# Performance work log

Hardware: AMD Instinct MI355X
Metric: run time of the kernel (lower is better)

## Reference

```python
import jax, jax.numpy as jnp
import numpy as np

TAU = 0.05
SIGMA = 0.05
THETA = 1.0
MAX_ITER = 30
B, N, M1, M2 = 8192, 256, 128, 64


def setup_inputs() -> dict:
    key = jax.random.key(0)
    k = jax.random.split(key, 5)
    x0 = jax.random.normal(k[0], (B, N), dtype=jnp.float32)
    y1_0 = jnp.zeros((B, M1), dtype=jnp.float32)
    y2_0 = jnp.zeros((B, M2), dtype=jnp.float32)
    z = jax.random.normal(k[1], (B, M1 + M2), dtype=jnp.float32)
    c = jax.random.normal(k[2], (N,), dtype=jnp.float32)
    # scale constraint matrices so tau*sigma*||A||^2 < 1 (PDHG stability)
    A1 = jax.random.normal(k[3], (M1, N), dtype=jnp.float32) * 0.1
    A2 = jax.random.normal(k[4], (M2, N), dtype=jnp.float32) * 0.1
    return {"x0": x0, "y1_0": y1_0, "y2_0": y2_0, "z": z, "c": c, "A1": A1, "A2": A2}


def reference(x0, y1_0, y2_0, z, c, A1, A2):
    # affine constraint maps: ineq_map(x, z) = x @ A1^T - z1 ; eq_map(x, z) = x @ A2^T - z2
    # adjoints: A1^T y1 = y1 @ A1 ; A2^T y2 = y2 @ A2
    # prox: projection onto nonnegative orthant
    z1, z2 = z[:, :M1], z[:, M1:]

    def step(carry, _):
        x, x_bar, y1, y2 = carry
        y1 = jnp.maximum(y1 + SIGMA * (x_bar @ A1.T - z1), 0.0)   # dual ineq ascent + clamp
        y2 = y2 + SIGMA * (x_bar @ A2.T - z2)                     # dual eq ascent
        grad = c + y1 @ A1 + y2 @ A2                              # [B, N] via broadcast of c
        x_next = jnp.maximum(x - TAU * grad, 0.0)                 # prox (nonneg projection)
        x_bar = x_next + THETA * (x_next - x)                     # extrapolation
        return (x_next, x_bar, y1, y2), None

    (x, _, y1, y2), _ = jax.lax.scan(step, (x0, x0, y1_0, y2_0), None, length=MAX_ITER)
    return (x, y1, y2)
```

## Files before the change

kernel.cpp:

```cpp
#include <hip/hip_runtime.h>

typedef __attribute__((ext_vector_type(8))) __bf16 bf16x8;
typedef __attribute__((ext_vector_type(4))) float f32x4;
typedef __attribute__((ext_vector_type(4))) int i32x4;

constexpr int Bn = 8192, Nn = 256, M1n = 128, M2n = 64, Mn = 192, ITERS = 30;
constexpr float TAUc = 0.05f, SIGc = 0.05f;

__device__ __forceinline__ ushort f2bf(float f) {
  unsigned u = __builtin_bit_cast(unsigned, f);
  u = (u + 0x7FFFu + ((u >> 16) & 1u)) >> 16;
  return (ushort)u;
}

__device__ __forceinline__ unsigned cvtpk(float lo, float hi) {
  unsigned r;
  asm("v_cvt_pk_bf16_f32 %0, %1, %2" : "=v"(r) : "v"(lo), "v"(hi));
  return r;
}

__device__ __forceinline__ void pina(i32x4& v) { asm volatile("" : "+a"(v)); }

__device__ __forceinline__ f32x4 mfma_b(bf16x8 a, i32x4 bfrag, f32x4 acc) {
  return __builtin_amdgcn_mfma_f32_16x16x32_bf16(
      a, __builtin_bit_cast(bf16x8, bfrag), acc, 0, 0, 0);
}

__global__ void prep_kernel(const float* __restrict__ A1, const float* __restrict__ A2,
                            ushort* __restrict__ Arm, ushort* __restrict__ AT) {
  int i = blockIdx.x * 256 + threadIdx.x;
  if (i >= Mn * Nn) return;
  int m = i / Nn, n = i % Nn;
  float v = (m < M1n) ? A1[m * Nn + n] : A2[(m - M1n) * Nn + n];
  ushort b = f2bf(v);
  Arm[m * Nn + n] = b;
  AT[n * Mn + m] = b;
}

__global__ __launch_bounds__(512, 2) void pdhg_kernel(
    const float* __restrict__ x0, const float* __restrict__ y10,
    const float* __restrict__ y20, const float* __restrict__ z,
    const float* __restrict__ c, const ushort* __restrict__ Arm,
    const ushort* __restrict__ AT, float* __restrict__ out) {
  __shared__ __align__(16) ushort xb_lds[2][16][264];
  __shared__ __align__(16) ushort y_lds[2][16][200];

  const int lane = threadIdx.x & 63;
  const int w = threadIdx.x >> 6;
  const int fr = lane & 15;
  const int kg = lane >> 4;
  const int row0 = blockIdx.x * 32;

  const int m01 = w * 16 + fr;
  const int m2 = M1n + (w & 3) * 16 + fr;
  const int bu2 = w >> 2;
  const int nA = (2 * w) * 16 + fr;
  const int nB = (2 * w + 1) * 16 + fr;

  float x[2][2][4];
  float yu[3][4], zu[3][4];
  const float cvA = c[nA], cvB = c[nB];

#pragma unroll
  for (int t = 0; t < 2; ++t) {
    const int n = t ? nB : nA;
#pragma unroll
    for (int b = 0; b < 2; ++b)
#pragma unroll
      for (int g = 0; g < 4; ++g) {
        float v = x0[(row0 + 16 * b + kg * 4 + g) * Nn + n];
        x[t][b][g] = v;
        xb_lds[b][kg * 4 + g][n] = f2bf(v);
      }
  }
#pragma unroll
  for (int g = 0; g < 4; ++g) {
    int r0 = row0 + kg * 4 + g;
    int r1 = r0 + 16;
    int r2 = row0 + 16 * bu2 + kg * 4 + g;
    zu[0][g] = SIGc * z[r0 * Mn + m01];  yu[0][g] = y10[r0 * M1n + m01];
    zu[1][g] = SIGc * z[r1 * Mn + m01];  yu[1][g] = y10[r1 * M1n + m01];
    zu[2][g] = SIGc * z[r2 * Mn + m2];   yu[2][g] = y20[r2 * M2n + (m2 - M1n)];
  }

  i32x4 armF01[8], armF2[8], atFA[6], atFB[6];
#pragma unroll
  for (int kf = 0; kf < 8; ++kf) {
    armF01[kf] = *reinterpret_cast<const i32x4*>(&Arm[m01 * Nn + kf * 32 + kg * 8]); pina(armF01[kf]);
    armF2[kf]  = *reinterpret_cast<const i32x4*>(&Arm[m2 * Nn + kf * 32 + kg * 8]);  pina(armF2[kf]);
  }
#pragma unroll
  for (int kf = 0; kf < 6; ++kf) {
    atFA[kf] = *reinterpret_cast<const i32x4*>(&AT[nA * Mn + kf * 32 + kg * 8]); pina(atFA[kf]);
    atFB[kf] = *reinterpret_cast<const i32x4*>(&AT[nB * Mn + kf * 32 + kg * 8]); pina(atFB[kf]);
  }

  __syncthreads();

  for (int it = 0; it < ITERS; ++it) {
    f32x4 a0 = {0.f, 0.f, 0.f, 0.f}, a1 = a0, a2 = a0;
#pragma unroll
    for (int kf = 0; kf < 8; ++kf) {
      bf16x8 f0 = *reinterpret_cast<const bf16x8*>(&xb_lds[0][fr][kf * 32 + kg * 8]);
      bf16x8 f1 = *reinterpret_cast<const bf16x8*>(&xb_lds[1][fr][kf * 32 + kg * 8]);
      bf16x8 f2 = *reinterpret_cast<const bf16x8*>(&xb_lds[bu2][fr][kf * 32 + kg * 8]);
      a0 = mfma_b(f0, armF01[kf], a0);
      a1 = mfma_b(f1, armF01[kf], a1);
      a2 = mfma_b(f2, armF2[kf], a2);
    }

#pragma unroll
    for (int g = 0; g < 4; ++g) {
      yu[0][g] = fmaxf(__builtin_fmaf(SIGc, a0[g], yu[0][g]) - zu[0][g], 0.f);
      yu[1][g] = fmaxf(__builtin_fmaf(SIGc, a1[g], yu[1][g]) - zu[1][g], 0.f);
      yu[2][g] = __builtin_fmaf(SIGc, a2[g], yu[2][g]) - zu[2][g];
    }
    {
      unsigned p01 = cvtpk(yu[0][0], yu[0][1]), p23 = cvtpk(yu[0][2], yu[0][3]);
      y_lds[0][kg * 4 + 0][m01] = (ushort)p01;
      y_lds[0][kg * 4 + 1][m01] = (ushort)(p01 >> 16);
      y_lds[0][kg * 4 + 2][m01] = (ushort)p23;
      y_lds[0][kg * 4 + 3][m01] = (ushort)(p23 >> 16);
    }
    {
      unsigned p01 = cvtpk(yu[1][0], yu[1][1]), p23 = cvtpk(yu[1][2], yu[1][3]);
      y_lds[1][kg * 4 + 0][m01] = (ushort)p01;
      y_lds[1][kg * 4 + 1][m01] = (ushort)(p01 >> 16);
      y_lds[1][kg * 4 + 2][m01] = (ushort)p23;
      y_lds[1][kg * 4 + 3][m01] = (ushort)(p23 >> 16);
    }
    {
      unsigned p01 = cvtpk(yu[2][0], yu[2][1]), p23 = cvtpk(yu[2][2], yu[2][3]);
      y_lds[bu2][kg * 4 + 0][m2] = (ushort)p01;
      y_lds[bu2][kg * 4 + 1][m2] = (ushort)(p01 >> 16);
      y_lds[bu2][kg * 4 + 2][m2] = (ushort)p23;
      y_lds[bu2][kg * 4 + 3][m2] = (ushort)(p23 >> 16);
    }
    __syncthreads();

    f32x4 b00 = {0.f, 0.f, 0.f, 0.f}, b01 = b00, b10 = b00, b11 = b00;
#pragma unroll
    for (int kf = 0; kf < 6; ++kf) {
      bf16x8 g0 = *reinterpret_cast<const bf16x8*>(&y_lds[0][fr][kf * 32 + kg * 8]);
      bf16x8 g1 = *reinterpret_cast<const bf16x8*>(&y_lds[1][fr][kf * 32 + kg * 8]);
      b00 = mfma_b(g0, atFA[kf], b00);
      b01 = mfma_b(g0, atFB[kf], b01);
      b10 = mfma_b(g1, atFA[kf], b10);
      b11 = mfma_b(g1, atFB[kf], b11);
    }

    const bool notlast = (it != ITERS - 1);
#pragma unroll
    for (int t = 0; t < 2; ++t) {
      const int n = t ? nB : nA;
      const float cv = t ? cvB : cvA;
#pragma unroll
      for (int b = 0; b < 2; ++b) {
        const f32x4 bt = (t == 0) ? (b == 0 ? b00 : b10) : (b == 0 ? b01 : b11);
        float xb[4];
#pragma unroll
        for (int g = 0; g < 4; ++g) {
          float grad = cv + bt[g];
          float xn = fmaxf(__builtin_fmaf(-TAUc, grad, x[t][b][g]), 0.f);
          xb[g] = 2.f * xn - x[t][b][g];
          x[t][b][g] = xn;
        }
        if (notlast) {
          unsigned p01 = cvtpk(xb[0], xb[1]), p23 = cvtpk(xb[2], xb[3]);
          xb_lds[b][kg * 4 + 0][n] = (ushort)p01;
          xb_lds[b][kg * 4 + 1][n] = (ushort)(p01 >> 16);
          xb_lds[b][kg * 4 + 2][n] = (ushort)p23;
          xb_lds[b][kg * 4 + 3][n] = (ushort)(p23 >> 16);
        }
      }
    }
    if (notlast) __syncthreads();
  }

  float* ox = out;
  float* oy1 = out + Bn * Nn;
  float* oy2 = oy1 + Bn * M1n;
#pragma unroll
  for (int t = 0; t < 2; ++t) {
    const int n = t ? nB : nA;
#pragma unroll
    for (int b = 0; b < 2; ++b)
#pragma unroll
      for (int g = 0; g < 4; ++g)
        ox[(row0 + 16 * b + kg * 4 + g) * Nn + n] = x[t][b][g];
  }
#pragma unroll
  for (int g = 0; g < 4; ++g) {
    int r0 = row0 + kg * 4 + g;
    oy1[r0 * M1n + m01] = yu[0][g];
    oy1[(r0 + 16) * M1n + m01] = yu[1][g];
    oy2[(row0 + 16 * bu2 + kg * 4 + g) * M2n + (m2 - M1n)] = yu[2][g];
  }
}

extern "C" void kernel_launch(void* const* d_in, const int* in_sizes, int n_in,
                              void* d_out, int out_size, void* d_ws, size_t ws_size,
                              hipStream_t stream) {
  const float* x0  = (const float*)d_in[0];
  const float* y10 = (const float*)d_in[1];
  const float* y20 = (const float*)d_in[2];
  const float* z   = (const float*)d_in[3];
  const float* c   = (const float*)d_in[4];
  const float* A1  = (const float*)d_in[5];
  const float* A2  = (const float*)d_in[6];

  ushort* Arm = (ushort*)d_ws;
  ushort* AT  = Arm + Mn * Nn;

  prep_kernel<<<(Mn * Nn + 255) / 256, 256, 0, stream>>>(A1, A2, Arm, AT);
  pdhg_kernel<<<Bn / 32, 512, 0, stream>>>(x0, y10, y20, z, c, Arm, AT, (float*)d_out);
}
```

Measured before the change: 74.13 us.

## Swap MFMA operands so outputs are row-contiguous and vectorize LDS/global I/O

Swaps the MFMA A/B operands so the register-resident A-matrix fragments are the A operand and the activations are B. Each lane's accumulator then holds four consecutive columns of one batch row instead of four rows of one column. This lets LDS writes of x_bar and y become single 8-byte stores instead of four 2-byte scattered stores, and makes the initial loads and final stores 16-byte vectors. It also changes the warp work split to 3 M-tiles by 1 batch tile in the first GEMM, which reduces redundant LDS reads of x_bar. Bank conflicts from the new row-strided store pattern are a possible risk.

```diff
diff --git a/kernel.cpp b/kernel.cpp
--- a/kernel.cpp
+++ b/kernel.cpp
@@ -21,9 +21,9 @@
 
 __device__ __forceinline__ void pina(i32x4& v) { asm volatile("" : "+a"(v)); }
 
-__device__ __forceinline__ f32x4 mfma_b(bf16x8 a, i32x4 bfrag, f32x4 acc) {
+__device__ __forceinline__ f32x4 mfma_swp(i32x4 afrag, bf16x8 b, f32x4 acc) {
   return __builtin_amdgcn_mfma_f32_16x16x32_bf16(
-      a, __builtin_bit_cast(bf16x8, bfrag), acc, 0, 0, 0);
+      __builtin_bit_cast(bf16x8, afrag), b, acc, 0, 0, 0);
 }
 
 __global__ void prep_kernel(const float* __restrict__ A1, const float* __restrict__ A2,
@@ -51,48 +51,56 @@
   const int kg = lane >> 4;
   const int row0 = blockIdx.x * 32;
 
-  const int m01 = w * 16 + fr;
-  const int m2 = M1n + (w & 3) * 16 + fr;
-  const int bu2 = w >> 2;
-  const int nA = (2 * w) * 16 + fr;
-  const int nB = (2 * w + 1) * 16 + fr;
+  const int b1 = w & 1;
+  const int mg = w >> 1;
+  const int rG1 = row0 + 16 * b1 + fr;
 
   float x[2][2][4];
-  float yu[3][4], zu[3][4];
-  const float cvA = c[nA], cvB = c[nB];
+  float cv[2][4];
+  float ys[3][4], zs[3][4];
 
 #pragma unroll
   for (int t = 0; t < 2; ++t) {
-    const int n = t ? nB : nA;
-#pragma unroll
-    for (int b = 0; b < 2; ++b)
-#pragma unroll
-      for (int g = 0; g < 4; ++g) {
-        float v = x0[(row0 + 16 * b + kg * 4 + g) * Nn + n];
-        x[t][b][g] = v;
-        xb_lds[b][kg * 4 + g][n] = f2bf(v);
-      }
-  }
-#pragma unroll
-  for (int g = 0; g < 4; ++g) {
-    int r0 = row0 + kg * 4 + g;
-    int r1 = r0 + 16;
-    int r2 = row0 + 16 * bu2 + kg * 4 + g;
-    zu[0][g] = SIGc * z[r0 * Mn + m01];  yu[0][g] = y10[r0 * M1n + m01];
-    zu[1][g] = SIGc * z[r1 * Mn + m01];  yu[1][g] = y10[r1 * M1n + m01];
-    zu[2][g] = SIGc * z[r2 * Mn + m2];   yu[2][g] = y20[r2 * M2n + (m2 - M1n)];
-  }
-
-  i32x4 armF01[8], armF2[8], atFA[6], atFB[6];
-#pragma unroll
-  for (int kf = 0; kf < 8; ++kf) {
-    armF01[kf] = *reinterpret_cast<const i32x4*>(&Arm[m01 * Nn + kf * 32 + kg * 8]); pina(armF01[kf]);
-    armF2[kf]  = *reinterpret_cast<const i32x4*>(&Arm[m2 * Nn + kf * 32 + kg * 8]);  pina(armF2[kf]);
-  }
-#pragma unroll
-  for (int kf = 0; kf < 6; ++kf) {
-    atFA[kf] = *reinterpret_cast<const i32x4*>(&AT[nA * Mn + kf * 32 + kg * 8]); pina(atFA[kf]);
-    atFB[kf] = *reinterpret_cast<const i32x4*>(&AT[nB * Mn + kf * 32 + kg * 8]); pina(atFB[kf]);
+    const int n0 = (2 * w + t) * 16 + kg * 4;
+    *reinterpret_cast<f32x4*>(cv[t]) = *reinterpret_cast<const f32x4*>(&c[n0]);
+#pragma unroll
+    for (int b = 0; b < 2; ++b) {
+      f32x4 v = *reinterpret_cast<const f32x4*>(&x0[(row0 + 16 * b + fr) * Nn + n0]);
+#pragma unroll
+      for (int g = 0; g < 4; ++g) x[t][b][g] = v[g];
+      uint2 p = make_uint2(cvtpk(v[0], v[1]), cvtpk(v[2], v[3]));
+      *reinterpret_cast<uint2*>(&xb_lds[b][fr][n0]) = p;
+    }
+  }
+#pragma unroll
+  for (int i = 0; i < 3; ++i) {
+    const int mt = 3 * mg + i;
+    const int m0 = mt * 16 + kg * 4;
+    f32x4 zv = *reinterpret_cast<const f32x4*>(&z[rG1 * Mn + m0]);
+    f32x4 yv = (mt < 8) ? *reinterpret_cast<const f32x4*>(&y10[rG1 * M1n + m0])
+                        : *reinterpret_cast<const f32x4*>(&y20[rG1 * M2n + (m0 - M1n)]);
+#pragma unroll
+    for (int g = 0; g < 4; ++g) { zs[i][g] = SIGc * zv[g]; ys[i][g] = yv[g]; }
+  }
+
+  i32x4 armF[3][8], atF[2][6];
+#pragma unroll
+  for (int i = 0; i < 3; ++i) {
+    const int m = (3 * mg + i) * 16 + fr;
+#pragma unroll
+    for (int kf = 0; kf < 8; ++kf) {
+      armF[i][kf] = *reinterpret_cast<const i32x4*>(&Arm[m * Nn + kf * 32 + kg * 8]);
+      pina(armF[i][kf]);
+    }
+  }
+#pragma unroll
+  for (int t = 0; t < 2; ++t) {
+    const int n = (2 * w + t) * 16 + fr;
+#pragma unroll
+    for (int kf = 0; kf < 6; ++kf) {
+      atF[t][kf] = *reinterpret_cast<const i32x4*>(&AT[n * Mn + kf * 32 + kg * 8]);
+      pina(atF[t][kf]);
+    }
   }
 
   __syncthreads();
@@ -101,76 +109,57 @@
     f32x4 a0 = {0.f, 0.f, 0.f, 0.f}, a1 = a0, a2 = a0;
 #pragma unroll
     for (int kf = 0; kf < 8; ++kf) {
-      bf16x8 f0 = *reinterpret_cast<const bf16x8*>(&xb_lds[0][fr][kf * 32 + kg * 8]);
-      bf16x8 f1 = *reinterpret_cast<const bf16x8*>(&xb_lds[1][fr][kf * 32 + kg * 8]);
-      bf16x8 f2 = *reinterpret_cast<const bf16x8*>(&xb_lds[bu2][fr][kf * 32 + kg * 8]);
-      a0 = mfma_b(f0, armF01[kf], a0);
-      a1 = mfma_b(f1, armF01[kf], a1);
-      a2 = mfma_b(f2, armF2[kf], a2);
-    }
-
-#pragma unroll
-    for (int g = 0; g < 4; ++g) {
-      yu[0][g] = fmaxf(__builtin_fmaf(SIGc, a0[g], yu[0][g]) - zu[0][g], 0.f);
-      yu[1][g] = fmaxf(__builtin_fmaf(SIGc, a1[g], yu[1][g]) - zu[1][g], 0.f);
-      yu[2][g] = __builtin_fmaf(SIGc, a2[g], yu[2][g]) - zu[2][g];
-    }
-    {
-      unsigned p01 = cvtpk(yu[0][0], yu[0][1]), p23 = cvtpk(yu[0][2], yu[0][3]);
-      y_lds[0][kg * 4 + 0][m01] = (ushort)p01;
-      y_lds[0][kg * 4 + 1][m01] = (ushort)(p01 >> 16);
-      y_lds[0][kg * 4 + 2][m01] = (ushort)p23;
-      y_lds[0][kg * 4 + 3][m01] = (ushort)(p23 >> 16);
-    }
-    {
-      unsigned p01 = cvtpk(yu[1][0], yu[1][1]), p23 = cvtpk(yu[1][2], yu[1][3]);
-      y_lds[1][kg * 4 + 0][m01] = (ushort)p01;
-      y_lds[1][kg * 4 + 1][m01] = (ushort)(p01 >> 16);
-      y_lds[1][kg * 4 + 2][m01] = (ushort)p23;
-      y_lds[1][kg * 4 + 3][m01] = (ushort)(p23 >> 16);
-    }
-    {
-      unsigned p01 = cvtpk(yu[2][0], yu[2][1]), p23 = cvtpk(yu[2][2], yu[2][3]);
-      y_lds[bu2][kg * 4 + 0][m2] = (ushort)p01;
-      y_lds[bu2][kg * 4 + 1][m2] = (ushort)(p01 >> 16);
-      y_lds[bu2][kg * 4 + 2][m2] = (ushort)p23;
-      y_lds[bu2][kg * 4 + 3][m2] = (ushort)(p23 >> 16);
+      bf16x8 fx = *reinterpret_cast<const bf16x8*>(&xb_lds[b1][fr][kf * 32 + kg * 8]);
+      a0 = mfma_swp(armF[0][kf], fx, a0);
+      a1 = mfma_swp(armF[1][kf], fx, a1);
+      a2 = mfma_swp(armF[2][kf], fx, a2);
+    }
+
+#pragma unroll
+    for (int i = 0; i < 3; ++i) {
+      const int mt = 3 * mg + i;
+      const int m0 = mt * 16 + kg * 4;
+      const f32x4 ai = (i == 0) ? a0 : (i == 1) ? a1 : a2;
+      const bool relu = (mt < 8);
+#pragma unroll
+      for (int g = 0; g < 4; ++g) {
+        float s = __builtin_fmaf(SIGc, ai[g], ys[i][g]) - zs[i][g];
+        ys[i][g] = relu ? fmaxf(s, 0.f) : s;
+      }
+      uint2 p = make_uint2(cvtpk(ys[i][0], ys[i][1]), cvtpk(ys[i][2], ys[i][3]));
+      *reinterpret_cast<uint2*>(&y_lds[b1][fr][m0]) = p;
     }
     __syncthreads();
 
-    f32x4 b00 = {0.f, 0.f, 0.f, 0.f}, b01 = b00, b10 = b00, b11 = b00;
+    f32x4 q00 = {0.f, 0.f, 0.f, 0.f}, q01 = q00, q10 = q00, q11 = q00;
 #pragma unroll
     for (int kf = 0; kf < 6; ++kf) {
       bf16x8 g0 = *reinterpret_cast<const bf16x8*>(&y_lds[0][fr][kf * 32 + kg * 8]);
       bf16x8 g1 = *reinterpret_cast<const bf16x8*>(&y_lds[1][fr][kf * 32 + kg * 8]);
-      b00 = mfma_b(g0, atFA[kf], b00);
-      b01 = mfma_b(g0, atFB[kf], b01);
-      b10 = mfma_b(g1, atFA[kf], b10);
-      b11 = mfma_b(g1, atFB[kf], b11);
+      q00 = mfma_swp(atF[0][kf], g0, q00);
+      q01 = mfma_swp(atF[1][kf], g0, q01);
+      q10 = mfma_swp(atF[0][kf], g1, q10);
+      q11 = mfma_swp(atF[1][kf], g1, q11);
     }
 
     const bool notlast = (it != ITERS - 1);
 #pragma unroll
     for (int t = 0; t < 2; ++t) {
-      const int n = t ? nB : nA;
-      const float cv = t ? cvB : cvA;
+      const int n0 = (2 * w + t) * 16 + kg * 4;
 #pragma unroll
       for (int b = 0; b < 2; ++b) {
-        const f32x4 bt = (t == 0) ? (b == 0 ? b00 : b10) : (b == 0 ? b01 : b11);
+        const f32x4 qt = (t == 0) ? (b == 0 ? q00 : q10) : (b == 0 ? q01 : q11);
         float xb[4];
 #pragma unroll
         for (int g = 0; g < 4; ++g) {
-          float grad = cv + bt[g];
+          float grad = cv[t][g] + qt[g];
           float xn = fmaxf(__builtin_fmaf(-TAUc, grad, x[t][b][g]), 0.f);
           xb[g] = 2.f * xn - x[t][b][g];
           x[t][b][g] = xn;
         }
         if (notlast) {
-          unsigned p01 = cvtpk(xb[0], xb[1]), p23 = cvtpk(xb[2], xb[3]);
-          xb_lds[b][kg * 4 + 0][n] = (ushort)p01;
-          xb_lds[b][kg * 4 + 1][n] = (ushort)(p01 >> 16);
-          xb_lds[b][kg * 4 + 2][n] = (ushort)p23;
-          xb_lds[b][kg * 4 + 3][n] = (ushort)(p23 >> 16);
+          uint2 p = make_uint2(cvtpk(xb[0], xb[1]), cvtpk(xb[2], xb[3]));
+          *reinterpret_cast<uint2*>(&xb_lds[b][fr][n0]) = p;
         }
       }
     }
@@ -182,19 +171,24 @@
   float* oy2 = oy1 + Bn * M1n;
 #pragma unroll
   for (int t = 0; t < 2; ++t) {
-    const int n = t ? nB : nA;
-#pragma unroll
-    for (int b = 0; b < 2; ++b)
-#pragma unroll
-      for (int g = 0; g < 4; ++g)
-        ox[(row0 + 16 * b + kg * 4 + g) * Nn + n] = x[t][b][g];
-  }
-#pragma unroll
-  for (int g = 0; g < 4; ++g) {
-    int r0 = row0 + kg * 4 + g;
-    oy1[r0 * M1n + m01] = yu[0][g];
-    oy1[(r0 + 16) * M1n + m01] = yu[1][g];
-    oy2[(row0 + 16 * bu2 + kg * 4 + g) * M2n + (m2 - M1n)] = yu[2][g];
+    const int n0 = (2 * w + t) * 16 + kg * 4;
+#pragma unroll
+    for (int b = 0; b < 2; ++b) {
+      f32x4 v;
+#pragma unroll
+      for (int g = 0; g < 4; ++g) v[g] = x[t][b][g];
+      *reinterpret_cast<f32x4*>(&ox[(row0 + 16 * b + fr) * Nn + n0]) = v;
+    }
+  }
+#pragma unroll
+  for (int i = 0; i < 3; ++i) {
+    const int mt = 3 * mg + i;
+    const int m0 = mt * 16 + kg * 4;
+    f32x4 v;
+#pragma unroll
+    for (int g = 0; g < 4; ++g) v[g] = ys[i][g];
+    if (mt < 8) *reinterpret_cast<f32x4*>(&oy1[rG1 * M1n + m0]) = v;
+    else        *reinterpret_cast<f32x4*>(&oy2[rG1 * M2n + (m0 - M1n)]) = v;
   }
 }
 
```

Result: faster. 67.69 us (-8.7%).
